# Optimization experiments

Measured on AMD Instinct MI355X. Metric: run time of the kernel, lower is better.

## Reference

```python
import jax, jax.numpy as jnp
import numpy as np

B, S, H, KVH, D = 1, 2048, 32, 8, 128
ROPE_THETA = 500000.0


def _rotate_half(x):
    x1, x2 = jnp.split(x, 2, axis=-1)
    return jnp.concatenate((-x2, x1), axis=-1)


def setup_inputs() -> dict:
    key = jax.random.key(0)
    ks = jax.random.split(key, 5)
    hidden_states = jax.random.normal(ks[0], (B, S, H * D), dtype=jnp.float32)
    Wq = jax.random.normal(ks[1], (H * D, H * D), dtype=jnp.float32) * 0.02
    Wk = jax.random.normal(ks[2], (KVH * D, H * D), dtype=jnp.float32) * 0.02
    Wv = jax.random.normal(ks[3], (KVH * D, H * D), dtype=jnp.float32) * 0.02
    Wo = jax.random.normal(ks[4], (H * D, H * D), dtype=jnp.float32) * 0.02
    # rotary tables (Llama-style, concat of freqs with itself)
    inv_freq = 1.0 / (ROPE_THETA ** (jnp.arange(0, D, 2, dtype=jnp.float32) / D))
    freqs = jnp.arange(S, dtype=jnp.float32)[:, None] * inv_freq[None, :]  # [S, D/2]
    emb = jnp.concatenate((freqs, freqs), axis=-1)  # [S, D]
    cos = jnp.cos(emb)[None]  # [1, S, D]
    sin = jnp.sin(emb)[None]
    # additive causal mask, matching SDPA attn_mask semantics
    causal = jnp.tril(jnp.ones((S, S), dtype=bool))
    attention_mask = jnp.where(causal, 0.0, -1e9).astype(jnp.float32)[None, None]  # [1,1,S,S]
    return {"hidden_states": hidden_states, "attention_mask": attention_mask,
            "cos": cos, "sin": sin, "Wq": Wq, "Wk": Wk, "Wv": Wv, "Wo": Wo}


def reference(hidden_states, attention_mask, cos, sin, Wq, Wk, Wv, Wo):
    b, s, _ = hidden_states.shape
    d = cos.shape[-1]
    h = Wq.shape[0] // d
    kvh = Wk.shape[0] // d
    g = h // kvh  # GQA group size

    # fused QKV projection (nn.Linear: y = x @ W^T), then split heads -> [b, heads, s, d]
    q = jnp.einsum('bsi,oi->bso', hidden_states, Wq).reshape(b, s, h, d).transpose(0, 2, 1, 3)
    k = jnp.einsum('bsi,oi->bso', hidden_states, Wk).reshape(b, s, kvh, d).transpose(0, 2, 1, 3)
    v = jnp.einsum('bsi,oi->bso', hidden_states, Wv).reshape(b, s, kvh, d).transpose(0, 2, 1, 3)

    # rotary embedding (unsqueeze_dim=1)
    c = cos[:, None]  # [b,1,s,d]
    sn = sin[:, None]
    q = q * c + _rotate_half(q) * sn
    k = k * c + _rotate_half(k) * sn

    # GQA: view q as [b, kvh, g, s, d]; contract against un-repeated k/v
    qg = q.reshape(b, kvh, g, s, d)
    scale = 1.0 / jnp.sqrt(jnp.float32(d))
    scores = jnp.einsum('bkgsd,bktd->bkgst', qg, k) * scale  # [b,kvh,g,s,s]
    scores = scores + attention_mask[:, :, None]  # broadcast [b,1,1,s,s]
    probs = jax.nn.softmax(scores, axis=-1)
    attn = jnp.einsum('bkgst,bktd->bkgsd', probs, v)  # [b,kvh,g,s,d]

    attn = attn.reshape(b, h, s, d).transpose(0, 2, 1, 3).reshape(b, s, h * d)
    out = jnp.einsum('bso,po->bsp', attn, Wo)
    return out
```

## Files before the change

kernel.cpp:

```cpp
#include <hip/hip_runtime.h>
#include <hip/hip_bf16.h>

#define SEQ 2048
#define HD  128
#define NH  32
#define NKV 8
#define MODEL 4096
#define KVDIM 1024
#define QKVN 6144

typedef __attribute__((ext_vector_type(8))) short short8;
typedef __attribute__((ext_vector_type(4))) short short4v;
typedef __attribute__((ext_vector_type(4))) float float4v;

#define MFMA16(a, b, c) __builtin_amdgcn_mfma_f32_16x16x32_bf16(a, b, c, 0, 0, 0)

__device__ __forceinline__ short f2bf(float x) {
  unsigned u = __builtin_bit_cast(unsigned, x);
  u += 0x7fffu + ((u >> 16) & 1u);
  return (short)(u >> 16);
}
__device__ __forceinline__ float bf2f(short s) {
  unsigned u = ((unsigned)(unsigned short)s) << 16;
  return __builtin_bit_cast(float, u);
}

__device__ __forceinline__ void async_copy16(const void* g, void* l) {
  __builtin_amdgcn_global_load_lds((const __attribute__((address_space(1))) void*)g,
                                   (__attribute__((address_space(3))) void*)l, 16, 0, 0);
}

__global__ __launch_bounds__(256) void cast_bf16(const float* __restrict__ in,
                                                 short* __restrict__ out, int n) {
  int i = (blockIdx.x * 256 + threadIdx.x) * 4;
  if (i < n) {
    float4v v = *(const float4v*)(in + i);
    short4v o;
    o[0] = f2bf(v[0]); o[1] = f2bf(v[1]); o[2] = f2bf(v[2]); o[3] = f2bf(v[3]);
    *(short4v*)(out + i) = o;
  }
}

#define BM 128
#define BN 128
#define BK 32

__device__ __forceinline__ void store_out(float* C, size_t idx, float v) { C[idx] = v; }
__device__ __forceinline__ void store_out(short* C, size_t idx, float v) { C[idx] = f2bf(v); }

template <typename OUT>
__global__ __launch_bounds__(256) void gemm_nt(const short* __restrict__ A,
                                               const short* __restrict__ B,
                                               OUT* __restrict__ C,
                                               int M, int N, int K) {
  __shared__ __align__(16) short As[2][BM * BK];
  __shared__ __align__(16) short Bs[2][BN * BK];
  int t = threadIdx.x;
  int w = t >> 6, lane = t & 63;
  int col = lane & 15, quad = lane >> 4;
  int m0 = blockIdx.y * BM, n0 = blockIdx.x * BN;
  int wr = (w >> 1) * 64, wc = (w & 1) * 64;

  int srow   = lane >> 2;
  int schunk = (lane & 3) ^ ((lane >> 3) & 3);
  const short* Ag0 = A + (size_t)(m0 + w * 32 + srow) * K + schunk * 8;
  const short* Ag1 = Ag0 + (size_t)16 * K;
  const short* Bg0 = B + (size_t)(n0 + w * 32 + srow) * K + schunk * 8;
  const short* Bg1 = Bg0 + (size_t)16 * K;
  const int wofs0 = (w * 32) * BK;
  const int wofs1 = (w * 32 + 16) * BK;

  int aswz = (quad ^ ((col >> 1) & 3)) * 8;

  float4v acc[4][4] = {};

  async_copy16(Ag0, &As[0][wofs0]);
  async_copy16(Ag1, &As[0][wofs1]);
  async_copy16(Bg0, &Bs[0][wofs0]);
  async_copy16(Bg1, &Bs[0][wofs1]);
  __syncthreads();

  const int iters = K / BK;
  for (int it = 0; it < iters; it++) {
    const int cb = it & 1, nb = cb ^ 1;
    if (it + 1 < iters) {
      const int k0 = (it + 1) * BK;
      async_copy16(Ag0 + k0, &As[nb][wofs0]);
      async_copy16(Ag1 + k0, &As[nb][wofs1]);
      async_copy16(Bg0 + k0, &Bs[nb][wofs0]);
      async_copy16(Bg1 + k0, &Bs[nb][wofs1]);
    }
    short8 af[4], bfr[4];
#pragma unroll
    for (int i = 0; i < 4; i++)
      af[i] = *(const short8*)&As[cb][(wr + i * 16 + col) * BK + aswz];
#pragma unroll
    for (int i = 0; i < 4; i++)
      bfr[i] = *(const short8*)&Bs[cb][(wc + i * 16 + col) * BK + aswz];
#pragma unroll
    for (int mi = 0; mi < 4; mi++)
#pragma unroll
      for (int ni = 0; ni < 4; ni++)
        acc[mi][ni] = MFMA16(af[mi], bfr[ni], acc[mi][ni]);
    __syncthreads();
  }

#pragma unroll
  for (int mi = 0; mi < 4; mi++)
#pragma unroll
    for (int ni = 0; ni < 4; ni++)
#pragma unroll
      for (int r = 0; r < 4; r++) {
        int row = m0 + wr + mi * 16 + quad * 4 + r;
        int cc  = n0 + wc + ni * 16 + col;
        store_out(C, (size_t)row * N + cc, acc[mi][ni][r]);
      }
}

__global__ __launch_bounds__(128) void rope_kernel(const short* __restrict__ qkv,
                                                   const float* __restrict__ cosp,
                                                   const float* __restrict__ sinp,
                                                   short* __restrict__ qb,
                                                   short* __restrict__ kb) {
  int s = blockIdx.x, head = blockIdx.y, d = threadIdx.x;
  float c  = cosp[s * HD + d];
  float sn = sinp[s * HD + d];
  if (head < NH) {
    const short* base = qkv + (size_t)s * QKVN + head * HD;
    float x = bf2f(base[d]);
    float rot = (d < 64) ? -bf2f(base[d + 64]) : bf2f(base[d - 64]);
    qb[((size_t)(head * SEQ + s)) * HD + d] = f2bf((x * c + rot * sn) * 0.08838834764831845f);
  } else {
    int hk = head - NH;
    const short* base = qkv + (size_t)s * QKVN + MODEL + hk * HD;
    float x = bf2f(base[d]);
    float rot = (d < 64) ? -bf2f(base[d + 64]) : bf2f(base[d - 64]);
    kb[((size_t)(hk * SEQ + s)) * HD + d] = f2bf(x * c + rot * sn);
  }
}

__global__ __launch_bounds__(256) void vtrans_kernel(const short* __restrict__ qkv,
                                                     short* __restrict__ vt) {
  __shared__ short tile[32][34];
  int kv = blockIdx.z;
  int d0 = blockIdx.x * 32, s0 = blockIdx.y * 32;
  int tx = threadIdx.x, ty = threadIdx.y;
#pragma unroll
  for (int j = 0; j < 32; j += 8)
    tile[ty + j][tx] = qkv[(size_t)(s0 + ty + j) * QKVN + MODEL + KVDIM + kv * HD + d0 + tx];
  __syncthreads();
#pragma unroll
  for (int j = 0; j < 32; j += 8)
    vt[((size_t)(kv * HD + d0 + ty + j)) * SEQ + s0 + tx] = tile[tx][ty + j];
}

#define FKT 32
#define KLD 136
#define VLD 40
#define PLD 40

__global__ __launch_bounds__(256, 3) void flash_attn(const short* __restrict__ qb_,
                                                     const short* __restrict__ kb,
                                                     const short* __restrict__ vt,
                                                     short* __restrict__ attn) {
  __shared__ __align__(16) short Ks[2][FKT * KLD];
  __shared__ __align__(16) short Vs[2][HD * VLD];
  __shared__ __align__(16) short Ps[4][32 * PLD];
  const int tid = threadIdx.x;
  const int w = tid >> 6, lane = tid & 63;
  const int col = lane & 15, quad = lane >> 4;
  const int h = blockIdx.x;
  const int kv = h >> 2;
  const int yp = (blockIdx.y < 8) ? (15 - (int)blockIdx.y) : ((int)blockIdx.y - 8);
  const int qB0 = yp * 128;
  const int q0w = qB0 + w * 32;
  const int ntiles = qB0 / FKT + 4;

  short8 ones;
#pragma unroll
  for (int i = 0; i < 8; i++) ones[i] = (short)0x3F80;

  short8 qf[2][4];
  const short* qbase = qb_ + ((size_t)(h * SEQ + q0w + col)) * HD;
#pragma unroll
  for (int rt = 0; rt < 2; rt++)
#pragma unroll
    for (int ks = 0; ks < 4; ks++)
      qf[rt][ks] = *(const short8*)(qbase + rt * 16 * HD + ks * 32 + quad * 8);

  float4v o[2][8] = {};
  float4v la[2] = {};

  const int kg_off = tid * 8;
  const int klds0  = (kg_off >> 7) * KLD + (kg_off & 127);
  const int vd     = tid >> 2;
  const int vkof   = (tid & 3) * 8;
  const size_t vrow0 = ((size_t)(kv * HD + vd)) * SEQ;
  const size_t vrow1 = ((size_t)(kv * HD + vd + 64)) * SEQ;
  const int vlds0 = vd * VLD + vkof;
  const short* kgbase = kb + ((size_t)kv * SEQ) * HD;

  short8 kr0, kr1, vr0, vr1;
  kr0 = *(const short8*)(kgbase + kg_off);
  kr1 = *(const short8*)(kgbase + 2048 + kg_off);
  vr0 = *(const short8*)(vt + vrow0 + vkof);
  vr1 = *(const short8*)(vt + vrow1 + vkof);
  *(short8*)&Ks[0][klds0]            = kr0;
  *(short8*)&Ks[0][klds0 + 16 * KLD] = kr1;
  *(short8*)&Vs[0][vlds0]            = vr0;
  *(short8*)&Vs[0][vlds0 + 64 * VLD] = vr1;
  __syncthreads();

  for (int kt = 0; kt < ntiles; kt++) {
    const int b = kt & 1;
    const int key0 = kt * FKT;
    if (kt + 1 < ntiles) {
      const int nk0 = key0 + FKT;
      const short* kg = kgbase + (size_t)nk0 * HD;
      kr0 = *(const short8*)(kg + kg_off);
      kr1 = *(const short8*)(kg + 2048 + kg_off);
      vr0 = *(const short8*)(vt + vrow0 + nk0 + vkof);
      vr1 = *(const short8*)(vt + vrow1 + nk0 + vkof);
    }
    if (key0 <= q0w + 31) {
      float4v sct[2][2] = {};
#pragma unroll
      for (int ks = 0; ks < 4; ks++) {
        short8 kf0 = *(const short8*)&Ks[b][col * KLD + ks * 32 + quad * 8];
        short8 kf1 = *(const short8*)&Ks[b][(16 + col) * KLD + ks * 32 + quad * 8];
        sct[0][0] = MFMA16(kf0, qf[0][ks], sct[0][0]);
        sct[0][1] = MFMA16(kf0, qf[1][ks], sct[0][1]);
        sct[1][0] = MFMA16(kf1, qf[0][ks], sct[1][0]);
        sct[1][1] = MFMA16(kf1, qf[1][ks], sct[1][1]);
      }
      short* pw = Ps[w];
#pragma unroll
      for (int rt = 0; rt < 2; rt++) {
        int qrow = q0w + rt * 16 + col;
#pragma unroll
        for (int kt2 = 0; kt2 < 2; kt2++) {
          int keyb = key0 + kt2 * 16 + quad * 4;
          short4v p;
#pragma unroll
          for (int r = 0; r < 4; r++) {
            float s = sct[kt2][rt][r];
            if (keyb + r > qrow) s = -INFINITY;
            p[r] = f2bf(__expf(s));
          }
          *(short4v*)&pw[(rt * 16 + col) * PLD + kt2 * 16 + quad * 4] = p;
        }
      }
      asm volatile("s_waitcnt lgkmcnt(0)" ::: "memory");
      short8 pf0 = *(const short8*)&pw[col * PLD + quad * 8];
      short8 pf1 = *(const short8*)&pw[(16 + col) * PLD + quad * 8];
      la[0] = MFMA16(ones, pf0, la[0]);
      la[1] = MFMA16(ones, pf1, la[1]);
#pragma unroll
      for (int nc = 0; nc < 8; nc++) {
        short8 vb = *(const short8*)&Vs[b][(nc * 16 + col) * VLD + quad * 8];
        o[0][nc] = MFMA16(vb, pf0, o[0][nc]);
        o[1][nc] = MFMA16(vb, pf1, o[1][nc]);
      }
    }
    if (kt + 1 < ntiles) {
      const int nb = 1 - b;
      *(short8*)&Ks[nb][klds0]            = kr0;
      *(short8*)&Ks[nb][klds0 + 16 * KLD] = kr1;
      *(short8*)&Vs[nb][vlds0]            = vr0;
      *(short8*)&Vs[nb][vlds0 + 64 * VLD] = vr1;
    }
    __syncthreads();
  }

#pragma unroll
  for (int rt = 0; rt < 2; rt++) {
    float inv = 1.0f / la[rt][0];
    size_t rowbase = (size_t)(q0w + rt * 16 + col) * MODEL + h * HD + quad * 4;
#pragma unroll
    for (int nc = 0; nc < 8; nc++) {
      short4v ov;
#pragma unroll
      for (int r = 0; r < 4; r++) ov[r] = f2bf(o[rt][nc][r] * inv);
      *(short4v*)(attn + rowbase + nc * 16) = ov;
    }
  }
}

extern "C" void kernel_launch(void* const* d_in, const int* in_sizes, int n_in,
                              void* d_out, int out_size, void* d_ws, size_t ws_size,
                              hipStream_t stream) {
  const float* hidden = (const float*)d_in[0];
  const float* cosp = (const float*)d_in[2];
  const float* sinp = (const float*)d_in[3];
  const float* Wq   = (const float*)d_in[4];
  const float* Wk   = (const float*)d_in[5];
  const float* Wv   = (const float*)d_in[6];
  const float* Wo   = (const float*)d_in[7];

  char* ws = (char*)d_ws;
  size_t off = 0;
  auto alloc = [&](size_t bytes) {
    char* p = ws + off;
    off += (bytes + 255) & ~(size_t)255;
    return p;
  };
  short* wq_bf = (short*)alloc((size_t)MODEL * MODEL * 2);
  short* wk_bf = (short*)alloc((size_t)KVDIM * MODEL * 2);
  short* wv_bf = (short*)alloc((size_t)KVDIM * MODEL * 2);
  short* wo_bf = (short*)alloc((size_t)MODEL * MODEL * 2);
  short* h_bf  = (short*)alloc((size_t)SEQ * MODEL * 2);
  short* qkv_bf = (short*)alloc((size_t)SEQ * QKVN * 2);
  short* k_bf  = (short*)alloc((size_t)NKV * SEQ * HD * 2);
  short* v_t   = (short*)alloc((size_t)NKV * HD * SEQ * 2);
  short* attn_bf = (short*)alloc((size_t)SEQ * MODEL * 2);
  short* q_bf    = h_bf;

  {
    int n;
    n = SEQ * MODEL;    cast_bf16<<<n / 1024, 256, 0, stream>>>(hidden, h_bf, n);
    n = MODEL * MODEL;  cast_bf16<<<n / 1024, 256, 0, stream>>>(Wq, wq_bf, n);
    n = KVDIM * MODEL;  cast_bf16<<<n / 1024, 256, 0, stream>>>(Wk, wk_bf, n);
    n = KVDIM * MODEL;  cast_bf16<<<n / 1024, 256, 0, stream>>>(Wv, wv_bf, n);
    n = MODEL * MODEL;  cast_bf16<<<n / 1024, 256, 0, stream>>>(Wo, wo_bf, n);
  }

  gemm_nt<short><<<dim3(QKVN / BN, SEQ / BM), 256, 0, stream>>>(h_bf, wq_bf, qkv_bf, SEQ, QKVN, MODEL);

  rope_kernel<<<dim3(SEQ, NH + NKV), 128, 0, stream>>>(qkv_bf, cosp, sinp, q_bf, k_bf);
  vtrans_kernel<<<dim3(HD / 32, SEQ / 32, NKV), dim3(32, 8), 0, stream>>>(qkv_bf, v_t);

  flash_attn<<<dim3(NH, SEQ / 128), 256, 0, stream>>>(q_bf, k_bf, v_t, attn_bf);

  gemm_nt<float><<<dim3(MODEL / BN, SEQ / BM), 256, 0, stream>>>(attn_bf, wo_bf, (float*)d_out, SEQ, MODEL, MODEL);
}
```

Measured before the change: 521.4 us.

## Add 256x256-tile pipelined GEMM for the fused QKV projection

Replaces the 128x128 tile QKV projection GEMM with a new 512-thread kernel that computes 256x256 tiles with BK=64. It uses async global-to-LDS loads with an XOR-swizzled layout, interleaved prefetch of the next k-tile between MFMA phases, setprio hints and a grouped block swizzle for L2 locality. The aim is more data reuse per LDS load and better overlap of memory with MFMA work. The cost is more LDS per block (128KB) and fewer blocks (192) to fill the GPU.

```diff
diff --git a/kernel.cpp b/kernel.cpp
--- a/kernel.cpp
+++ b/kernel.cpp
@@ -39,6 +39,153 @@
     o[0] = f2bf(v[0]); o[1] = f2bf(v[1]); o[2] = f2bf(v[2]); o[3] = f2bf(v[3]);
     *(short4v*)(out + i) = o;
   }
+}
+
+__global__ __launch_bounds__(512, 2) void gemm256(const short* __restrict__ A,
+                                                  const short* __restrict__ B,
+                                                  short* __restrict__ C,
+                                                  int M, int N, int K) {
+  __shared__ __align__(16) short As[2][256 * 64];
+  __shared__ __align__(16) short Bs[2][256 * 64];
+  const int tid = threadIdx.x;
+  const int lane = tid & 63, w = tid >> 6;
+  const int col = lane & 15, quad = lane >> 4;
+  const int wm = w >> 2, wn = w & 3;
+
+  const int nbx = N >> 8;
+  int bid = blockIdx.x, nwg = gridDim.x;
+  int swz = (nwg & 7) ? bid : ((bid & 7) * (nwg >> 3) + (bid >> 3));
+  const int m0 = (swz / nbx) << 8;
+  const int n0 = (swz % nbx) << 8;
+
+  const int srow = tid >> 3;
+  const int schunk = (tid & 7) ^ (srow & 7);
+  const short* pA = A + (size_t)(m0 + srow) * K + schunk * 8;
+  const short* pB = B + (size_t)(n0 + srow) * K + schunk * 8;
+  const int ldst = tid * 8;
+
+  const int sw = (col & 7) << 3;
+  const int kof0 = (quad * 8) ^ sw;
+  const int kof1 = (32 + quad * 8) ^ sw;
+  const int ra = wm * 128, rb = wn * 64;
+
+  float4v acc[8][4] = {};
+  const int iters = K >> 6;
+
+#define SA(buf, rA, kt) async_copy16(pA + (size_t)(rA) * K + (kt), &As[buf][(rA) * 64 + ldst])
+#define SB_(buf, rB, kt) async_copy16(pB + (size_t)(rB) * K + (kt), &Bs[buf][(rB) * 64 + ldst])
+
+  SA(0, 0, 0);  SA(0, 128, 0);
+  SB_(0, 0, 0); SB_(0, 64, 0); SB_(0, 128, 0); SB_(0, 192, 0);
+  SA(0, 64, 0); SA(0, 192, 0);
+  asm volatile("s_waitcnt vmcnt(2)" ::: "memory");
+  __builtin_amdgcn_s_barrier();
+
+  for (int t = 0; t < iters; ++t) {
+    const int cb = t & 1, nb = cb ^ 1;
+    const int kt = (t + 1) << 6;
+    const bool pf = (t + 1 < iters);
+    const short* a_ = As[cb];
+    const short* b_ = Bs[cb];
+    short8 af[4][2], bf0[2][2], bf1[2][2];
+
+#pragma unroll
+    for (int mi = 0; mi < 4; ++mi) {
+      const short* rp = a_ + (ra + mi * 16 + col) * 64;
+      af[mi][0] = *(const short8*)(rp + kof0);
+      af[mi][1] = *(const short8*)(rp + kof1);
+    }
+#pragma unroll
+    for (int ni = 0; ni < 2; ++ni) {
+      const short* rp = b_ + (rb + ni * 16 + col) * 64;
+      bf0[ni][0] = *(const short8*)(rp + kof0);
+      bf0[ni][1] = *(const short8*)(rp + kof1);
+    }
+    if (pf) { SA(nb, 0, kt); SA(nb, 128, kt); }
+    __builtin_amdgcn_s_barrier();
+    asm volatile("s_waitcnt lgkmcnt(0)" ::: "memory");
+    __builtin_amdgcn_sched_barrier(0);
+    __builtin_amdgcn_s_setprio(1);
+#pragma unroll
+    for (int mi = 0; mi < 4; ++mi)
+#pragma unroll
+      for (int ni = 0; ni < 2; ++ni) {
+        acc[mi][ni] = MFMA16(af[mi][0], bf0[ni][0], acc[mi][ni]);
+        acc[mi][ni] = MFMA16(af[mi][1], bf0[ni][1], acc[mi][ni]);
+      }
+    __builtin_amdgcn_s_setprio(0);
+    __builtin_amdgcn_s_barrier();
+
+#pragma unroll
+    for (int ni = 0; ni < 2; ++ni) {
+      const short* rp = b_ + (rb + (ni + 2) * 16 + col) * 64;
+      bf1[ni][0] = *(const short8*)(rp + kof0);
+      bf1[ni][1] = *(const short8*)(rp + kof1);
+    }
+    if (pf) { SB_(nb, 0, kt); SB_(nb, 64, kt); }
+    __builtin_amdgcn_s_barrier();
+    asm volatile("s_waitcnt lgkmcnt(0)" ::: "memory");
+    __builtin_amdgcn_sched_barrier(0);
+    __builtin_amdgcn_s_setprio(1);
+#pragma unroll
+    for (int mi = 0; mi < 4; ++mi)
+#pragma unroll
+      for (int ni = 0; ni < 2; ++ni) {
+        acc[mi][ni + 2] = MFMA16(af[mi][0], bf1[ni][0], acc[mi][ni + 2]);
+        acc[mi][ni + 2] = MFMA16(af[mi][1], bf1[ni][1], acc[mi][ni + 2]);
+      }
+    __builtin_amdgcn_s_setprio(0);
+    if (pf) asm volatile("s_waitcnt vmcnt(4)" ::: "memory");
+    else    asm volatile("s_waitcnt vmcnt(0)" ::: "memory");
+    __builtin_amdgcn_s_barrier();
+
+#pragma unroll
+    for (int mi = 0; mi < 4; ++mi) {
+      const short* rp = a_ + (ra + (mi + 4) * 16 + col) * 64;
+      af[mi][0] = *(const short8*)(rp + kof0);
+      af[mi][1] = *(const short8*)(rp + kof1);
+    }
+    if (pf) { SB_(nb, 128, kt); SB_(nb, 192, kt); }
+    __builtin_amdgcn_s_barrier();
+    asm volatile("s_waitcnt lgkmcnt(0)" ::: "memory");
+    __builtin_amdgcn_sched_barrier(0);
+    __builtin_amdgcn_s_setprio(1);
+#pragma unroll
+    for (int mi = 0; mi < 4; ++mi)
+#pragma unroll
+      for (int ni = 0; ni < 2; ++ni) {
+        acc[mi + 4][ni + 2] = MFMA16(af[mi][0], bf1[ni][0], acc[mi + 4][ni + 2]);
+        acc[mi + 4][ni + 2] = MFMA16(af[mi][1], bf1[ni][1], acc[mi + 4][ni + 2]);
+      }
+    __builtin_amdgcn_s_setprio(0);
+    __builtin_amdgcn_s_barrier();
+
+    if (pf) { SA(nb, 64, kt); SA(nb, 192, kt); }
+    __builtin_amdgcn_s_setprio(1);
+#pragma unroll
+    for (int mi = 0; mi < 4; ++mi)
+#pragma unroll
+      for (int ni = 0; ni < 2; ++ni) {
+        acc[mi + 4][ni] = MFMA16(af[mi][0], bf0[ni][0], acc[mi + 4][ni]);
+        acc[mi + 4][ni] = MFMA16(af[mi][1], bf0[ni][1], acc[mi + 4][ni]);
+      }
+    __builtin_amdgcn_s_setprio(0);
+    if (pf) asm volatile("s_waitcnt vmcnt(2)" ::: "memory");
+    __builtin_amdgcn_s_barrier();
+  }
+#undef SA
+#undef SB_
+
+#pragma unroll
+  for (int mi = 0; mi < 8; ++mi)
+#pragma unroll
+    for (int ni = 0; ni < 4; ++ni)
+#pragma unroll
+      for (int r = 0; r < 4; ++r) {
+        int row = m0 + ra + mi * 16 + quad * 4 + r;
+        int cc  = n0 + rb + ni * 16 + col;
+        C[(size_t)row * N + cc] = f2bf(acc[mi][ni][r]);
+      }
 }
 
 #define BM 128
@@ -324,7 +471,7 @@
     n = MODEL * MODEL;  cast_bf16<<<n / 1024, 256, 0, stream>>>(Wo, wo_bf, n);
   }
 
-  gemm_nt<short><<<dim3(QKVN / BN, SEQ / BM), 256, 0, stream>>>(h_bf, wq_bf, qkv_bf, SEQ, QKVN, MODEL);
+  gemm256<<<dim3((SEQ / 256) * (QKVN / 256)), 512, 0, stream>>>(h_bf, wq_bf, qkv_bf, SEQ, QKVN, MODEL);
 
   rope_kernel<<<dim3(SEQ, NH + NKV), 128, 0, stream>>>(qkv_bf, cosp, sinp, q_bf, k_bf);
   vtrans_kernel<<<dim3(HD / 32, SEQ / 32, NKV), dim3(32, 8), 0, stream>>>(qkv_bf, v_t);
```

New measurement: 531.2 us. Within noise of the previous version (+1.9%).
